# Kernel optimization log

Hardware: AMD Instinct MI355X
Metric: run time of the kernel (lower is better)

Reference implementation:

```python
import jax, jax.numpy as jnp
import numpy as np

EP = 1e-4
EPMAX = 30.0
RTOL, ATOL = 1e-5, 1e-8  # torch.allclose defaults


def _safe(n):
    return jnp.where(n == 0, 1.0, n)


def _rigid_from_3(x):
    # x: (L, 3, 3) -> rot (L,3,3) rows e1,e2,e3 ; origin (L,3)
    x1, x2, x3 = x[:, 0], x[:, 1], x[:, 2]
    v1 = x3 - x2
    v2 = x1 - x2
    e1 = v1 / (jnp.linalg.norm(v1, axis=-1, keepdims=True) + 1e-3)
    u2 = v2 - e1 * jnp.einsum('ld,ld->l', e1, v2)[:, None]
    e2 = u2 / (jnp.linalg.norm(u2, axis=-1, keepdims=True) + 1e-8)
    e3 = jnp.cross(e1, e2)
    return jnp.stack([e1, e2, e3], axis=1), x2


def _merge_frames(rot, trans, ii, jj):
    # Vectorized merge_coordinate_systems over all selected pairs (ii, jj).
    O_A, O_B = trans[ii], trans[jj]          # (P,3)
    RA, RB = rot[ii], rot[jj]                # (P,3,3)
    close = jnp.all(jnp.abs(O_A - O_B) <= ATOL + RTOL * jnp.abs(O_B), axis=-1)
    d = O_B - O_A
    nd = jnp.linalg.norm(d, axis=-1)
    X_new = d / _safe(nd)[:, None]
    Z_add = RA[:, 2] + RB[:, 2]
    Z_sub = RA[:, 2] - RB[:, 2]
    na = jnp.linalg.norm(Z_add, axis=-1)
    ns = jnp.linalg.norm(Z_sub, axis=-1)
    Z_new = jnp.where((na > ns)[:, None], Z_add / _safe(na)[:, None], Z_sub / _safe(ns)[:, None])
    Y_new = jnp.cross(Z_new, X_new)
    nan_bad = jnp.any(jnp.isnan(Y_new), axis=-1)
    flip = jnp.einsum('pd,pd->p', jnp.cross(X_new, Y_new), Z_new) < 0
    Y_new = jnp.where(flip[:, None], -Y_new, Y_new)
    R_new = jnp.stack([X_new, Y_new, Z_new], axis=1)  # (P,3,3)
    O_new = 0.5 * (O_A + O_B)
    bad = close | (nd == 0) | (na == 0) | (ns == 0) | nan_bad
    R_out = jnp.where(bad[:, None, None], RA, R_new)
    O_out = jnp.where(bad[:, None], O_A, O_new)
    return jnp.concatenate([rot, R_out], axis=0), jnp.concatenate([trans, O_out], axis=0)


def _frame_transform(points, rot, tran):
    # points: (N,3); rot: (F,3,3); tran: (F,3) -> (N,F,3)
    diff = points[:, None, :] - tran[None, :, :]
    return jnp.einsum('nfd,fed->nfe', diff, rot)


def setup_inputs():
    key = jax.random.key(0)
    k0, k1, k2, k3 = jax.random.split(key, 4)
    L = 1024
    coor = 5.0 * jax.random.normal(k0, (L, 3, 3), jnp.float32)
    # valid orthonormal frames from random points
    rot, _ = _rigid_from_3(5.0 * jax.random.normal(k1, (L, 3, 3), jnp.float32))
    trans = 5.0 * jax.random.normal(k2, (L, 3), jnp.float32)
    target = 5.0 * jax.random.normal(k3, (L, 3, 3), jnp.float32)
    idx = np.arange(L)
    band = idx[None, :] - idx[:, None]
    matrix = ((band > 0) & (band <= 8)).astype(np.int32)  # ~8k contact pairs
    return {"coor": coor, "rot": rot, "trans": trans, "target": target,
            "matrix": jnp.asarray(matrix)}


def reference(coor, rot, trans, target, matrix):
    m = np.asarray(matrix)
    ii_np, jj_np = np.nonzero(np.triu(m, 1) == 1)
    ii, jj = jnp.asarray(ii_np), jnp.asarray(jj_np)
    p_rot, p_tran = _merge_frames(rot, trans, ii, jj)
    pred_x2 = _frame_transform(coor.reshape(-1, 3), p_rot, p_tran)   # (N,F,3)
    t_rot0, t_tran0 = _rigid_from_3(target)
    t_rot, t_tran = _merge_frames(t_rot0, t_tran0, ii, jj)
    tx = _frame_transform(target.reshape(-1, 3), t_rot, t_tran)     # (N,F,3)
    errmap = jnp.sqrt(jnp.sum((pred_x2 - tx) ** 2 + EP, axis=-1))
    return jnp.mean(jnp.minimum(errmap, EPMAX))
```

## Files before the change

kernel.cpp:

```cpp
#include <hip/hip_runtime.h>

#define EPV    0.0001f
#define EPMAXV 30.0f
#define RTOLV  1e-5f
#define ATOLV  1e-8f
#define NPART  2048
#define FS     64


__device__ inline void write_rec(float* __restrict__ rec,
                                 const float Rp[9], const float Op[3],
                                 const float Rt[9], const float Ot[3]) {
    float P[9], N[9];
#pragma unroll
    for (int k = 0; k < 9; k++) { P[k] = Rp[k]; N[k] = -Rt[k]; }
    float kx = -(P[0] * Op[0] + P[1] * Op[1] + P[2] * Op[2]
               + N[0] * Ot[0] + N[1] * Ot[1] + N[2] * Ot[2]);
    float ky = -(P[3] * Op[0] + P[4] * Op[1] + P[5] * Op[2]
               + N[3] * Ot[0] + N[4] * Ot[1] + N[5] * Ot[2]);
    float kz = -(P[6] * Op[0] + P[7] * Op[1] + P[8] * Op[2]
               + N[6] * Ot[0] + N[7] * Ot[1] + N[8] * Ot[2]);
    float4* r4 = (float4*)rec;
    r4[0] = make_float4(P[0], P[1], P[2], P[3]);
    r4[1] = make_float4(P[4], P[5], P[6], P[7]);
    r4[2] = make_float4(P[8], N[0], N[1], N[2]);
    r4[3] = make_float4(N[3], N[4], N[5], N[6]);
    r4[4] = make_float4(N[7], N[8], kx, ky);
    r4[5] = make_float4(kz, 0.f, 0.f, 0.f);
}

__global__ void k_prep(const int* __restrict__ m, int L, unsigned int* __restrict__ rowcnt,
                       const float* __restrict__ rot, const float* __restrict__ trans,
                       const float* __restrict__ target, int nrb,
                       float* __restrict__ pF, float* __restrict__ tF,
                       float* __restrict__ rec) {
    if ((int)blockIdx.x < nrb) {
        int i = blockIdx.x * 4 + (threadIdx.x >> 6);
        if (i >= L) return;
        int lane = threadIdx.x & 63;
        const int* row = m + (size_t)i * L;
        unsigned int c = 0;
        for (int j0 = 0; j0 < L; j0 += 64) {
            int j = j0 + lane;
            bool v = (j < L) && (j > i) && (row[j] == 1);
            unsigned long long b = __ballot(v);
            c += (unsigned int)__popcll(b);
        }
        if (lane == 0) rowcnt[i] = c;
        return;
    }
    int l = ((int)blockIdx.x - nrb) * 256 + threadIdx.x;
    if (l >= L) return;
    float Rp[9], Op[3];
#pragma unroll
    for (int k = 0; k < 9; k++) Rp[k] = rot[l * 9 + k];
#pragma unroll
    for (int k = 0; k < 3; k++) Op[k] = trans[l * 3 + k];
    float* pf = pF + l * 12;
#pragma unroll
    for (int k = 0; k < 9; k++) pf[k] = Rp[k];
#pragma unroll
    for (int k = 0; k < 3; k++) pf[9 + k] = Op[k];
    const float* tg = target + l * 9;
    float x1x = tg[0], x1y = tg[1], x1z = tg[2];
    float x2x = tg[3], x2y = tg[4], x2z = tg[5];
    float x3x = tg[6], x3y = tg[7], x3z = tg[8];
    float v1x = x3x - x2x, v1y = x3y - x2y, v1z = x3z - x2z;
    float v2x = x1x - x2x, v2y = x1y - x2y, v2z = x1z - x2z;
    float n1 = sqrtf(v1x * v1x + v1y * v1y + v1z * v1z) + 0.001f;
    float e1x = v1x / n1, e1y = v1y / n1, e1z = v1z / n1;
    float c = e1x * v2x + e1y * v2y + e1z * v2z;
    float u2x = v2x - c * e1x, u2y = v2y - c * e1y, u2z = v2z - c * e1z;
    float n2 = sqrtf(u2x * u2x + u2y * u2y + u2z * u2z) + 1e-8f;
    float e2x = u2x / n2, e2y = u2y / n2, e2z = u2z / n2;
    float Rt[9], Ot[3];
    Rt[0] = e1x; Rt[1] = e1y; Rt[2] = e1z;
    Rt[3] = e2x; Rt[4] = e2y; Rt[5] = e2z;
    Rt[6] = e1y * e2z - e1z * e2y;
    Rt[7] = e1z * e2x - e1x * e2z;
    Rt[8] = e1x * e2y - e1y * e2x;
    Ot[0] = x2x; Ot[1] = x2y; Ot[2] = x2z;
    float* tf = tF + l * 12;
#pragma unroll
    for (int k = 0; k < 9; k++) tf[k] = Rt[k];
#pragma unroll
    for (int k = 0; k < 3; k++) tf[9 + k] = Ot[k];
    write_rec(rec + (size_t)l * 24, Rp, Op, Rt, Ot);
}

__device__ inline void merge_frames(const float* __restrict__ A, const float* __restrict__ B,
                                    float R[9], float O[3]) {
    const float* RA = A; const float* OA = A + 9;
    const float* RB = B; const float* OB = B + 9;
    bool close = (fabsf(OA[0] - OB[0]) <= ATOLV + RTOLV * fabsf(OB[0])) &&
                 (fabsf(OA[1] - OB[1]) <= ATOLV + RTOLV * fabsf(OB[1])) &&
                 (fabsf(OA[2] - OB[2]) <= ATOLV + RTOLV * fabsf(OB[2]));
    float d0 = OB[0] - OA[0], d1 = OB[1] - OA[1], d2 = OB[2] - OA[2];
    float nd = sqrtf(d0 * d0 + d1 * d1 + d2 * d2);
    float nds = (nd == 0.f) ? 1.f : nd;
    float X0 = d0 / nds, X1 = d1 / nds, X2 = d2 / nds;
    float Za0 = RA[6] + RB[6], Za1 = RA[7] + RB[7], Za2 = RA[8] + RB[8];
    float Zs0 = RA[6] - RB[6], Zs1 = RA[7] - RB[7], Zs2 = RA[8] - RB[8];
    float na = sqrtf(Za0 * Za0 + Za1 * Za1 + Za2 * Za2);
    float ns = sqrtf(Zs0 * Zs0 + Zs1 * Zs1 + Zs2 * Zs2);
    float nas = (na == 0.f) ? 1.f : na;
    float nss = (ns == 0.f) ? 1.f : ns;
    float Z0, Z1, Z2;
    if (na > ns) { Z0 = Za0 / nas; Z1 = Za1 / nas; Z2 = Za2 / nas; }
    else         { Z0 = Zs0 / nss; Z1 = Zs1 / nss; Z2 = Zs2 / nss; }
    float Y0 = Z1 * X2 - Z2 * X1;
    float Y1 = Z2 * X0 - Z0 * X2;
    float Y2 = Z0 * X1 - Z1 * X0;
    bool nanbad = (Y0 != Y0) || (Y1 != Y1) || (Y2 != Y2);
    float C0 = X1 * Y2 - X2 * Y1;
    float C1 = X2 * Y0 - X0 * Y2;
    float C2 = X0 * Y1 - X1 * Y0;
    float dotv = C0 * Z0 + C1 * Z1 + C2 * Z2;
    if (dotv < 0.f) { Y0 = -Y0; Y1 = -Y1; Y2 = -Y2; }
    bool bad = close || (nd == 0.f) || (na == 0.f) || (ns == 0.f) || nanbad;
    if (bad) {
#pragma unroll
        for (int k = 0; k < 9; k++) R[k] = RA[k];
#pragma unroll
        for (int k = 0; k < 3; k++) O[k] = OA[k];
    } else {
        R[0] = X0; R[1] = X1; R[2] = X2;
        R[3] = Y0; R[4] = Y1; R[5] = Y2;
        R[6] = Z0; R[7] = Z1; R[8] = Z2;
        O[0] = 0.5f * (OA[0] + OB[0]);
        O[1] = 0.5f * (OA[1] + OB[1]);
        O[2] = 0.5f * (OA[2] + OB[2]);
    }
}

__global__ void k_fillmerge(const int* __restrict__ m, int L,
                            const unsigned int* __restrict__ rowcnt,
                            unsigned int* __restrict__ count, int cap,
                            const float* __restrict__ pF, const float* __restrict__ tF,
                            float* __restrict__ rec) {
    int i = blockIdx.x * 4 + (threadIdx.x >> 6);
    int lane = threadIdx.x & 63;

    if (blockIdx.x == 0 && (threadIdx.x >> 6) == 0) {
        unsigned int t = 0;
        for (int r = lane; r < L; r += 64) t += rowcnt[r];
#pragma unroll
        for (int off = 1; off < 64; off <<= 1) t += __shfl_xor(t, off, 64);
        if (lane == 0) *count = t;
    }
    if (i >= L) return;

    unsigned int p = 0;
    for (int r = lane; r < i; r += 64) p += rowcnt[r];
#pragma unroll
    for (int off = 1; off < 64; off <<= 1) p += __shfl_xor(p, off, 64);
    unsigned int base = p;

    const int* row = m + (size_t)i * L;
    unsigned long long lt = (lane == 0) ? 0ull : ((1ull << lane) - 1ull);
    for (int j0 = 0; j0 < L; j0 += 64) {
        int j = j0 + lane;
        bool v = (j < L) && (j > i) && (row[j] == 1);
        unsigned long long b = __ballot(v);
        if (v) {
            unsigned int pos = base + (unsigned int)__popcll(b & lt);
            if (pos < (unsigned int)cap) {
                float Rp[9], Op[3], Rt[9], Ot[3];
                merge_frames(pF + i * 12, pF + j * 12, Rp, Op);
                merge_frames(tF + i * 12, tF + j * 12, Rt, Ot);
                write_rec(rec + (size_t)(L + pos) * 24, Rp, Op, Rt, Ot);
            }
        }
        base += (unsigned int)__popcll(b);
    }
}

__global__ __launch_bounds__(256)
void k_main(const float* __restrict__ coor, const float* __restrict__ target,
            const float* __restrict__ rec, const unsigned int* __restrict__ count,
            int cap, int L, int Npts, double* __restrict__ partials) {
    __shared__ float sRed[4];
    unsigned int cnt = *count;
    if (cnt > (unsigned int)cap) cnt = (unsigned int)cap;
    int F = L + (int)cnt;
    int npb = (Npts + 255) >> 8;
    int nfs = (F + FS - 1) / FS;
    int total = npb * nfs;
    float a0 = 0.f, a1 = 0.f;

    for (int chunk = blockIdx.x; chunk < total; chunk += gridDim.x) {
        int pb = chunk % npb;
        int fsI = chunk / npb;
        int pt = pb * 256 + threadIdx.x;
        bool alive = pt < Npts;
        int pi = alive ? pt * 3 : 0;
        float cx = coor[pi],   cy = coor[pi + 1],   cz = coor[pi + 2];
        float tx = target[pi], ty = target[pi + 1], tz = target[pi + 2];
        int f0 = fsI * FS;
        int f1 = f0 + FS; if (f1 > F) f1 = F;
        float b0 = 0.f, b1 = 0.f;
#pragma unroll 2
        for (int f = f0; f < f1; f++) {
            const float* fr = rec + (size_t)f * 24;
            float ux = fr[18] + fr[0] * cx + fr[1] * cy + fr[2] * cz
                               + fr[9] * tx + fr[10] * ty + fr[11] * tz;
            float uy = fr[19] + fr[3] * cx + fr[4] * cy + fr[5] * cz
                               + fr[12] * tx + fr[13] * ty + fr[14] * tz;
            float uz = fr[20] + fr[6] * cx + fr[7] * cy + fr[8] * cz
                               + fr[15] * tx + fr[16] * ty + fr[17] * tz;
            float s = ux * ux + uy * uy + uz * uz + 3.0f * EPV;
            float r = fminf(__builtin_amdgcn_sqrtf(s), EPMAXV);
            if (f & 1) b1 += r; else b0 += r;
        }
        if (alive) { a0 += b0; a1 += b1; }
    }

    float a = a0 + a1;
#pragma unroll
    for (int off = 32; off > 0; off >>= 1) a += __shfl_down(a, off, 64);
    int lane = threadIdx.x & 63, wv = threadIdx.x >> 6;
    if (lane == 0) sRed[wv] = a;
    __syncthreads();
    if (threadIdx.x == 0)
        partials[blockIdx.x] = (double)(sRed[0] + sRed[1] + sRed[2] + sRed[3]);
}

__global__ void k_final(const double* __restrict__ partials, int npart,
                        const unsigned int* __restrict__ count, int cap,
                        int L, int Npts, float* __restrict__ out) {
    __shared__ double sR[4];
    double d = 0.0;
    for (int i = threadIdx.x; i < npart; i += 256) d += partials[i];
#pragma unroll
    for (int off = 32; off > 0; off >>= 1) d += __shfl_down(d, off, 64);
    int lane = threadIdx.x & 63, wv = threadIdx.x >> 6;
    if (lane == 0) sR[wv] = d;
    __syncthreads();
    if (threadIdx.x == 0) {
        double tot = sR[0] + sR[1] + sR[2] + sR[3];
        unsigned int cnt = *count;
        if (cnt > (unsigned int)cap) cnt = (unsigned int)cap;
        double F = (double)(L + (int)cnt);
        out[0] = (float)(tot / ((double)Npts * F));
    }
}

extern "C" void kernel_launch(void* const* d_in, const int* in_sizes, int n_in,
                              void* d_out, int out_size, void* d_ws, size_t ws_size,
                              hipStream_t stream) {
    const float* coor   = (const float*)d_in[0];
    const float* rot    = (const float*)d_in[1];
    const float* trans  = (const float*)d_in[2];
    const float* target = (const float*)d_in[3];
    const int*   matrix = (const int*)d_in[4];
    int L    = in_sizes[2] / 3;
    int Npts = 3 * L;

    char* ws = (char*)d_ws;
    size_t off = 16;
    unsigned int* count  = (unsigned int*)ws;
    unsigned int* rowcnt = (unsigned int*)(ws + off); off += 4 * (size_t)L;
    off = (off + 15) & ~(size_t)15;
    double* partials = (double*)(ws + off); off += 8 * (size_t)NPART;
    off = (off + 15) & ~(size_t)15;
    float* pF = (float*)(ws + off); off += 48 * (size_t)L;
    float* tF = (float*)(ws + off); off += 48 * (size_t)L;
    off = (off + 15) & ~(size_t)15;
    long cap_ws = ((long)ws_size - (long)off - 96L * (long)L) / 96;
    long capl = cap_ws < 32768 ? cap_ws : 32768;
    if (capl < 0) capl = 0;
    int cap = (int)capl;
    float* rec = (float*)(ws + off);

    int nrb   = (L + 3) / 4;
    int nbase = (L + 255) / 256;
    k_prep<<<nrb + nbase, 256, 0, stream>>>(matrix, L, rowcnt, rot, trans, target,
                                            nrb, pF, tF, rec);
    k_fillmerge<<<nrb, 256, 0, stream>>>(matrix, L, rowcnt, count, cap, pF, tF, rec);
    k_main<<<NPART, 256, 0, stream>>>(coor, target, rec, count, cap, L, Npts, partials);
    k_final<<<1, 256, 0, stream>>>(partials, NPART, count, cap, L, Npts, (float*)d_out);
}
```

Measured before the change: 116.7 us.

## Map threads to frames and stage point chunks in LDS for k_main

The main loop is inverted. Each thread now owns one frame, holding its 21 transform coefficients in registers, and loops over a chunk of 112 points. Those points' coor/target coordinates are staged in shared memory as float4 and read as broadcasts. Previously each thread owned a point and streamed frame records from global memory. The change also lowers the partials count to 1024 and adds an occupancy hint to launch_bounds. The aim is to cut repeated per-frame global loads, in exchange for extra LDS traffic, block barriers, and idle threads in the last partial frame block.

```diff
diff --git a/kernel.cpp b/kernel.cpp
--- a/kernel.cpp
+++ b/kernel.cpp
@@ -4,8 +4,8 @@
 #define EPMAXV 30.0f
 #define RTOLV  1e-5f
 #define ATOLV  1e-8f
-#define NPART  2048
-#define FS     64
+#define NPART  1024
+#define CHUNK  112
 
 
 __device__ inline void write_rec(float* __restrict__ rec,
@@ -175,44 +175,60 @@
     }
 }
 
-__global__ __launch_bounds__(256)
+__global__ __launch_bounds__(256, 4)
 void k_main(const float* __restrict__ coor, const float* __restrict__ target,
             const float* __restrict__ rec, const unsigned int* __restrict__ count,
             int cap, int L, int Npts, double* __restrict__ partials) {
+    __shared__ float4 sC[CHUNK];
+    __shared__ float4 sT[CHUNK];
     __shared__ float sRed[4];
     unsigned int cnt = *count;
     if (cnt > (unsigned int)cap) cnt = (unsigned int)cap;
     int F = L + (int)cnt;
-    int npb = (Npts + 255) >> 8;
-    int nfs = (F + FS - 1) / FS;
-    int total = npb * nfs;
+    int nfb = (F + 255) >> 8;
+    int nyc = (Npts + CHUNK - 1) / CHUNK;
+    int total = nfb * nyc;
     float a0 = 0.f, a1 = 0.f;
 
     for (int chunk = blockIdx.x; chunk < total; chunk += gridDim.x) {
-        int pb = chunk % npb;
-        int fsI = chunk / npb;
-        int pt = pb * 256 + threadIdx.x;
-        bool alive = pt < Npts;
-        int pi = alive ? pt * 3 : 0;
-        float cx = coor[pi],   cy = coor[pi + 1],   cz = coor[pi + 2];
-        float tx = target[pi], ty = target[pi + 1], tz = target[pi + 2];
-        int f0 = fsI * FS;
-        int f1 = f0 + FS; if (f1 > F) f1 = F;
-        float b0 = 0.f, b1 = 0.f;
-#pragma unroll 2
-        for (int f = f0; f < f1; f++) {
-            const float* fr = rec + (size_t)f * 24;
-            float ux = fr[18] + fr[0] * cx + fr[1] * cy + fr[2] * cz
-                               + fr[9] * tx + fr[10] * ty + fr[11] * tz;
-            float uy = fr[19] + fr[3] * cx + fr[4] * cy + fr[5] * cz
-                               + fr[12] * tx + fr[13] * ty + fr[14] * tz;
-            float uz = fr[20] + fr[6] * cx + fr[7] * cy + fr[8] * cz
-                               + fr[15] * tx + fr[16] * ty + fr[17] * tz;
+        int fb = chunk % nfb;
+        int yc = chunk / nfb;
+        int n0 = yc * CHUNK;
+        int npts = Npts - n0; if (npts > CHUNK) npts = CHUNK;
+        __syncthreads();
+        for (int idx = threadIdx.x; idx < npts; idx += 256) {
+            int g = (n0 + idx) * 3;
+            sC[idx] = make_float4(coor[g], coor[g + 1], coor[g + 2], 0.f);
+            sT[idx] = make_float4(target[g], target[g + 1], target[g + 2], 0.f);
+        }
+        __syncthreads();
+        int f = fb * 256 + threadIdx.x;
+        if (f >= F) continue;
+
+        const float4* fr = (const float4*)(rec + (size_t)f * 24);
+        float4 r0 = fr[0], r1 = fr[1], r2 = fr[2], r3 = fr[3], r4 = fr[4], r5 = fr[5];
+        float P00 = r0.x, P01 = r0.y, P02 = r0.z;
+        float P10 = r0.w, P11 = r1.x, P12 = r1.y;
+        float P20 = r1.z, P21 = r1.w, P22 = r2.x;
+        float N00 = r2.y, N01 = r2.z, N02 = r2.w;
+        float N10 = r3.x, N11 = r3.y, N12 = r3.z;
+        float N20 = r3.w, N21 = r4.x, N22 = r4.y;
+        float kx  = r4.z, ky  = r4.w, kz  = r5.x;
+
+#pragma unroll 4
+        for (int n = 0; n < npts; n++) {
+            float4 c = sC[n];
+            float4 t = sT[n];
+            float ux = kx + P00 * c.x + P01 * c.y + P02 * c.z
+                          + N00 * t.x + N01 * t.y + N02 * t.z;
+            float uy = ky + P10 * c.x + P11 * c.y + P12 * c.z
+                          + N10 * t.x + N11 * t.y + N12 * t.z;
+            float uz = kz + P20 * c.x + P21 * c.y + P22 * c.z
+                          + N20 * t.x + N21 * t.y + N22 * t.z;
             float s = ux * ux + uy * uy + uz * uz + 3.0f * EPV;
             float r = fminf(__builtin_amdgcn_sqrtf(s), EPMAXV);
-            if (f & 1) b1 += r; else b0 += r;
-        }
-        if (alive) { a0 += b0; a1 += b1; }
+            if (n & 1) a1 += r; else a0 += r;
+        }
     }
 
     float a = a0 + a1;
```

Result: faster. 107.2 us (-8.1%).
